# Kernel optimization log

Measured on AMD Instinct MI355X. Metric: run time of the kernel, lower is better.

Reference implementation:

```python
import jax, jax.numpy as jnp
import numpy as np

B, H, W = 4, 768, 768
K = 4096            # max zero-crossing points kept per sample (padded/masked)
UPDATE_SCALE = 1.0
DIST_THRESHOLD = 3.0
W_INJECT = 1.0
W_PIXEL = 1.0
EPS = 1e-8
BIG = 1e30          # stand-in for +inf distance of invalid gt points


def _make_sdf(radius, center, key):
    # signed distance to a circle + smooth low-frequency perturbation -> realistic SDF
    r = jnp.arange(H, dtype=jnp.float32)[:, None]
    c = jnp.arange(W, dtype=jnp.float32)[None, :]
    d = jnp.sqrt((r - center[0]) ** 2 + (c - center[1]) ** 2) - radius
    noise = jax.random.normal(key, (H // 32, W // 32), dtype=jnp.float32)
    noise = jax.image.resize(noise, (H, W), method='bilinear') * 2.0
    return d + noise


def setup_inputs() -> dict:
    key = jax.random.key(0)
    ks = jax.random.split(key, 2 * B)
    preds, gts = [], []
    for b in range(B):
        cr, cc = H / 2 + 10 * b, W / 2 - 7 * b
        preds.append(_make_sdf(240.0 + 3 * b, (cr, cc), ks[2 * b]))
        gts.append(_make_sdf(250.0 - 2 * b, (cr + 5, cc - 4), ks[2 * b + 1]))
    return {"pred_sdf": jnp.stack(preds), "gt_sdf": jnp.stack(gts)}


def extract_zc(sdf):
    """Padded zero-crossing extraction: returns (K,2) coords and (K,) valid mask."""
    v1, v2 = sdf[:-1, :], sdf[1:, :]
    mask_v = (v1 * v2) < 0
    alpha_v = jnp.abs(v1) / (jnp.abs(v1) + jnp.abs(v2) + EPS)
    rs_v = jnp.arange(H - 1, dtype=jnp.float32)[:, None] + alpha_v          # (H-1,W)
    cs_v = jnp.broadcast_to(jnp.arange(W, dtype=jnp.float32)[None, :], (H - 1, W))

    h1, h2 = sdf[:, :-1], sdf[:, 1:]
    mask_h = (h1 * h2) < 0
    alpha_h = jnp.abs(h1) / (jnp.abs(h1) + jnp.abs(h2) + EPS)
    rs_h = jnp.broadcast_to(jnp.arange(H, dtype=jnp.float32)[:, None], (H, W - 1))
    cs_h = jnp.arange(W - 1, dtype=jnp.float32)[None, :] + alpha_h          # (H,W-1)

    mask_z = sdf == 0
    rz = jnp.broadcast_to(jnp.arange(H, dtype=jnp.float32)[:, None], (H, W))
    cz = jnp.broadcast_to(jnp.arange(W, dtype=jnp.float32)[None, :], (H, W))

    pts = jnp.concatenate([
        jnp.stack([rz.ravel(), cz.ravel()], -1),
        jnp.stack([rs_v.ravel(), cs_v.ravel()], -1),
        jnp.stack([rs_h.ravel(), cs_h.ravel()], -1)], axis=0)               # (M,2)
    mask = jnp.concatenate([mask_z.ravel(), mask_v.ravel(), mask_h.ravel()])
    order = jnp.argsort(~mask)[:K]      # stable sort -> True (crossing) entries first
    return pts[order], mask[order]


def compute_normals(sdf):
    gr = jnp.zeros_like(sdf)
    gr = gr.at[1:-1].set(0.5 * (sdf[2:] - sdf[:-2]))
    gr = gr.at[0].set(sdf[1] - sdf[0]).at[-1].set(sdf[-1] - sdf[-2])
    gc = jnp.zeros_like(sdf)
    gc = gc.at[:, 1:-1].set(0.5 * (sdf[:, 2:] - sdf[:, :-2]))
    gc = gc.at[:, 0].set(sdf[:, 1] - sdf[:, 0]).at[:, -1].set(sdf[:, -1] - sdf[:, -2])
    return jnp.stack([gr, gc], -1)      # (H,W,2)


def _corner(coords):
    r, c = coords[:, 0], coords[:, 1]
    r0 = jnp.clip(jnp.floor(r).astype(jnp.int32), 0, H - 1)
    c0 = jnp.clip(jnp.floor(c).astype(jnp.int32), 0, W - 1)
    r1 = jnp.clip(r0 + 1, 0, H - 1)
    c1 = jnp.clip(c0 + 1, 0, W - 1)
    ar = r - r0.astype(jnp.float32)
    ac = c - c0.astype(jnp.float32)
    return r0, c0, r1, c1, ar, ac


def bilinear_sample(img, coords):
    r0, c0, r1, c1, ar, ac = _corner(coords)
    return (img[r0, c0] * (1 - ar) * (1 - ac) + img[r0, c1] * (1 - ar) * ac
            + img[r1, c0] * ar * (1 - ac) + img[r1, c1] * ar * ac)


def chamfer_grad(pred2d, pred_zc, valid_p, gt_zc, valid_g):
    normals = compute_normals(pred2d)
    r0, c0, r1, c1, ar, ac = _corner(pred_zc)
    n = (normals[r0, c0] * ((1 - ar) * (1 - ac))[:, None]
         + normals[r0, c1] * ((1 - ar) * ac)[:, None]
         + normals[r1, c0] * (ar * (1 - ac))[:, None]
         + normals[r1, c1] * (ar * ac)[:, None])
    n = n / (jnp.linalg.norm(n, axis=1, keepdims=True) + 1e-8)

    diff = gt_zc[None, :, :] - pred_zc[:, None, :]          # (Kp,Kg,2)
    dist = jnp.linalg.norm(diff, axis=-1)                   # (Kp,Kg)
    dist = jnp.where(valid_g[None, :], dist, BIG)
    idx = jnp.argmin(dist, axis=1)
    min_dist = jnp.take_along_axis(dist, idx[:, None], 1)[:, 0]
    mask = (min_dist <= DIST_THRESHOLD) & valid_p & jnp.any(valid_g)
    dir_vec = jnp.take_along_axis(diff, idx[:, None, None], 1)[:, 0, :]
    dot = (dir_vec * n).sum(1) * UPDATE_SCALE
    dot = jnp.where(mask, dot, 0.0)

    w00 = (1 - ar) * (1 - ac); w01 = (1 - ar) * ac
    w10 = ar * (1 - ac);       w11 = ar * ac
    flat = lambda rr, cc: rr * W + cc
    indices = jnp.concatenate([flat(r0, c0), flat(r0, c1), flat(r1, c0), flat(r1, c1)])
    contribs = jnp.concatenate([dot * w00, dot * w01, dot * w10, dot * w11])
    dflat = jnp.zeros(H * W, dtype=pred2d.dtype).at[indices].add(contribs)
    return dflat.reshape(H, W)


def _per_sample(pred2d, gt2d):
    gt_zc, valid_g = extract_zc(gt2d)
    # torch uses pred.detach() for zero-crossing locations
    pred_zc, valid_p = extract_zc(jax.lax.stop_gradient(pred2d))
    dSDF = chamfer_grad(pred2d, pred_zc, valid_p, gt_zc, valid_g)
    inject = jnp.sum(pred2d * jax.lax.stop_gradient(dSDF))
    pixel = jnp.sum(jnp.where(valid_p, bilinear_sample(pred2d, pred_zc), 0.0))
    return inject, pixel


def reference(pred_sdf, gt_sdf):
    inject, pixel = jax.vmap(_per_sample)(pred_sdf, gt_sdf)
    return W_INJECT * inject.mean() + W_PIXEL * pixel.mean()
```

## Files before the change

kernel.cpp:

```cpp
#include <hip/hip_runtime.h>
#include <climits>


typedef unsigned long long ull;

constexpr int B = 4, H = 768, W = 768, K = 4096;
constexpr int HW = H * W;
constexpr int NFIELD = 2 * B;
constexpr int BANDS = 256;
constexpr int WPR = W / 64;
constexpr int SEGW = 768 * WPR;
constexpr int MSTRIDE = 3 * SEGW;
constexpr int GSPLIT = 16;
constexpr int GRNG = K / GSPLIT;
constexpr int IBLK = K / 256;
constexpr int NDBLK = B * HW / 256;
constexpr int NBKT_S = 16;

constexpr size_t alignup(size_t x, size_t a) { return (x + a - 1) & ~(a - 1); }

constexpr size_t OFF_ACCP  = 0;
constexpr size_t OFF_BACC  = OFF_ACCP + sizeof(double) * 8 * 8;
constexpr size_t OFF_CNT   = OFF_BACC + sizeof(double) * 64 * 8;
constexpr size_t OFF_WCNT  = OFF_CNT + sizeof(int) * NFIELD;
constexpr size_t OFF_MASKS = alignup(OFF_WCNT + sizeof(int) * NFIELD * 768, 8);
constexpr size_t OFF_PTS   = OFF_MASKS + sizeof(ull) * NFIELD * MSTRIDE;
constexpr size_t OFF_NNKEY = OFF_PTS + sizeof(float2) * NFIELD * K;
constexpr size_t OFF_HEADS = alignup(OFF_NNKEY + sizeof(ull) * (size_t)B * K, 16);
constexpr size_t OFF_NXT   = OFF_HEADS + sizeof(int) * (size_t)B * HW;
constexpr size_t OFF_EVAL  = OFF_NXT + sizeof(int) * (size_t)B * 4 * K;
constexpr size_t OFF_DIRTY = OFF_EVAL + sizeof(float) * (size_t)B * 4 * K;
constexpr size_t WS_NEED   = OFF_DIRTY + sizeof(int) * NDBLK;

#define DEVFN __device__ __forceinline__

DEVFN float grad_r(const float* __restrict__ s, int r, int c) {
#pragma clang fp contract(off)
  if (r == 0)      return s[W + c] - s[c];
  if (r == H - 1)  return s[(H - 1) * W + c] - s[(H - 2) * W + c];
  return 0.5f * (s[(r + 1) * W + c] - s[(r - 1) * W + c]);
}
DEVFN float grad_c(const float* __restrict__ s, int r, int c) {
#pragma clang fp contract(off)
  if (c == 0)      return s[r * W + 1] - s[r * W];
  if (c == W - 1)  return s[r * W + W - 1] - s[r * W + W - 2];
  return 0.5f * (s[r * W + c + 1] - s[r * W + c - 1]);
}

DEVFN const float* field_sdf(const float* pred, const float* gt, int f) {
  return ((f & 1) ? gt : pred) + (size_t)(f >> 1) * HW;
}

__global__ __launch_bounds__(256) void k_count(const float* __restrict__ pred,
                                               const float* __restrict__ gt,
                                               ull* __restrict__ masks,
                                               int* __restrict__ wave_cnt,
                                               int* __restrict__ heads,
                                               int* __restrict__ dirty,
                                               ull* __restrict__ nnkey,
                                               double* __restrict__ bacc,
                                               double* __restrict__ accp) {
#pragma clang fp contract(off)
  int gtid = blockIdx.x * 256 + (int)threadIdx.x;
  int gsz = gridDim.x * 256;
  int4* h4 = (int4*)heads;
  for (int idx = gtid; idx < B * HW / 4; idx += gsz)
    h4[idx] = make_int4(-1, -1, -1, -1);
  for (int idx = gtid; idx < NDBLK; idx += gsz) dirty[idx] = 0;
  for (int idx = gtid; idx < B * K; idx += gsz) nnkey[idx] = ~0ull;
  if (gtid < 64) accp[gtid] = 0.0;
  if (gtid >= 64 && gtid < 64 + 512) bacc[gtid - 64] = 0.0;

  int f = blockIdx.x >> 6;
  int bb = blockIdx.x & 63;
  int wave = threadIdx.x >> 6, lane = threadIdx.x & 63;
  int band = bb * 4 + wave;
  int r0 = band * 3;
  const float* sdf = field_sdf(pred, gt, f);
  ull* mz = masks + (size_t)f * MSTRIDE;
  ull* mv = mz + SEGW;
  ull* mh = mv + SEGW;

  float cur[WPR], nxt[WPR];
#pragma unroll
  for (int i = 0; i < WPR; ++i) cur[i] = sdf[r0 * W + i * 64 + lane];
  int cz = 0, cv = 0, ch = 0;
  for (int rr = 0; rr < 3; ++rr) {
    int row = r0 + rr;
    bool hasNext = row < H - 1;
    if (hasNext) {
#pragma unroll
      for (int i = 0; i < WPR; ++i) nxt[i] = sdf[(row + 1) * W + i * 64 + lane];
    }
#pragma unroll
    for (int i = 0; i < WPR; ++i) {
      ull m = __ballot(cur[i] == 0.0f);
      if (lane == 0) mz[row * WPR + i] = m;
      cz += __popcll(m);
      float nb = __shfl_down(cur[i], 1);
      float nb2 = (i < WPR - 1) ? __shfl(cur[i + 1], 0) : 0.0f;
      if (lane == 63) nb = nb2;
      bool hp = (i * 64 + lane < W - 1) && (cur[i] * nb < 0.0f);
      m = __ballot(hp);
      if (lane == 0) mh[row * WPR + i] = m;
      ch += __popcll(m);
      if (hasNext) {
        m = __ballot(cur[i] * nxt[i] < 0.0f);
        if (lane == 0) mv[row * WPR + i] = m;
        cv += __popcll(m);
      }
    }
    if (hasNext) {
#pragma unroll
      for (int i = 0; i < WPR; ++i) cur[i] = nxt[i];
    }
  }
  if (lane == 0) {
    int* wc = wave_cnt + f * 768;
    wc[0 * BANDS + band] = cz;
    wc[1 * BANDS + band] = cv;
    wc[2 * BANDS + band] = ch;
  }
}

__global__ __launch_bounds__(256) void k_emit(const float* __restrict__ pred,
                                              const float* __restrict__ gt,
                                              const ull* __restrict__ masks,
                                              const int* __restrict__ wave_cnt,
                                              float2* __restrict__ pts,
                                              int* __restrict__ counts_raw) {
#pragma clang fp contract(off)
  int f = blockIdx.x / 192;
  int tb = blockIdx.x - f * 192;
  __shared__ int cnt_s[768];
  for (int t = threadIdx.x; t < 768; t += 256) cnt_s[t] = wave_cnt[f * 768 + t];
  __syncthreads();
  int wave = threadIdx.x >> 6, lane = threadIdx.x & 63;
  int task = tb * 4 + wave;
  int seg = task >> 8, band = task & 255;
  int a = 0;
  for (int idx = lane; idx < task; idx += 64) a += cnt_s[idx];
  for (int off = 32; off > 0; off >>= 1) a += __shfl_xor(a, off, 64);
  int base = a;
  if (tb == 0 && wave == 0) {
    int t2 = 0;
    for (int idx = lane; idx < 768; idx += 64) t2 += cnt_s[idx];
    for (int off = 32; off > 0; off >>= 1) t2 += __shfl_xor(t2, off, 64);
    if (lane == 0) counts_raw[f] = t2;
  }
  if (base >= K) return;
  const float* sdf = field_sdf(pred, gt, f);
  const ull* mseg = masks + (size_t)f * MSTRIDE + (size_t)seg * SEGW;
  float2* fp = pts + (size_t)f * K;
  int r0 = band * 3;
  for (int rr = 0; rr < 3; ++rr) {
    int row = r0 + rr;
    if (seg == 1 && row >= H - 1) break;
    for (int i = 0; i < WPR; ++i) {
      ull m = mseg[row * WPR + i];
      if (!m) continue;
      if ((m >> lane) & 1ull) {
        int c = i * 64 + lane;
        float pr, pc;
        if (seg == 0) {
          pr = (float)row; pc = (float)c;
        } else if (seg == 1) {
          float v1 = sdf[row * W + c], v2 = sdf[(row + 1) * W + c];
          float a1 = fabsf(v1), a2 = fabsf(v2);
          float alpha = a1 / ((a1 + a2) + 1e-8f);
          pr = (float)row + alpha; pc = (float)c;
        } else {
          float h1 = sdf[row * W + c], h2 = sdf[row * W + c + 1];
          float a1 = fabsf(h1), a2 = fabsf(h2);
          float alpha = a1 / ((a1 + a2) + 1e-8f);
          pr = (float)row; pc = (float)c + alpha;
        }
        int pos = base + __popcll(m & ((1ull << lane) - 1ull));
        if (pos < K) fp[pos] = make_float2(pr, pc);
      }
      base += __popcll(m);
      if (base >= K) { rr = 3; break; }
    }
  }
}

__global__ __launch_bounds__(256) void k_nn(const float2* __restrict__ pts,
                                            const int* __restrict__ counts_raw,
                                            ull* __restrict__ nnkey) {
#pragma clang fp contract(off)
  int b = blockIdx.x >> 8;
  int rem = blockIdx.x & 255;
  int ib = rem >> 4, ig = rem & 15;
  int tid = (int)threadIdx.x;
  int np_ = min(counts_raw[2 * b + 0], K);
  int ng  = min(counts_raw[2 * b + 1], K);
  int j0 = ig * GRNG;
  int n = min(GRNG, ng - j0);
  const float2* gp = pts + (size_t)(2 * b + 1) * K;

  __shared__ float2 tile[GRNG];
  __shared__ float smin[256], smax[256];
  float rmin = __builtin_inff(), rmax = -__builtin_inff();
  if (tid < n) {
    float2 g = gp[j0 + tid];
    tile[tid] = g;
    rmin = g.x; rmax = g.x;
  }
  smin[tid] = rmin; smax[tid] = rmax;
  __syncthreads();
  for (int s = 128; s > 0; s >>= 1) {
    if (tid < s) {
      smin[tid] = fminf(smin[tid], smin[tid + s]);
      smax[tid] = fmaxf(smax[tid], smax[tid + s]);
    }
    __syncthreads();
  }
  float gmin = smin[0] - 3.001f, gmax = smax[0] + 3.001f;

  int i = ib * 256 + tid;
  if (i >= np_ || n <= 0) return;
  float2 q = pts[(size_t)(2 * b) * K + i];
  float pr = q.x, pc = q.y;
  if (pr < gmin || pr > gmax) return;
  float best = __builtin_inff();
  unsigned bj = 0xffffffffu;
#pragma unroll 4
  for (int j = 0; j < n; ++j) {
    float dr = tile[j].x - pr;
    float dc = tile[j].y - pc;
    float sqf = fmaf(dr, dr, dc * dc);
    if (sqf <= 9.0001f) {
      float d = sqrtf((dr * dr) + (dc * dc));
      if (d < best) { best = d; bj = (unsigned)(j0 + j); }
    }
  }
  if (bj != 0xffffffffu)
    atomicMin(&nnkey[(size_t)b * K + i],
              ((ull)__float_as_uint(best) << 32) | bj);
}

__global__ __launch_bounds__(256) void k_post(const float* __restrict__ pred,
                                              const float2* __restrict__ pts,
                                              const int* __restrict__ counts_raw,
                                              const ull* __restrict__ nnkey,
                                              int* __restrict__ heads,
                                              int* __restrict__ nxt,
                                              float* __restrict__ eval,
                                              int* __restrict__ dirty,
                                              double* __restrict__ accp) {
#pragma clang fp contract(off)
  int b = blockIdx.x >> 4;
  int i = ((blockIdx.x & 15) << 8) + (int)threadIdx.x;
  const float* P = pred + (size_t)b * HW;
  int np_ = min(counts_raw[2 * b + 0], K);
  bool active = (i < np_);
  float sval = 0.0f;
  if (active) {
    ull key = nnkey[(size_t)b * K + i];
    float2 q = pts[(size_t)(2 * b) * K + i];
    float pr = q.x, pc = q.y;

    int r0 = (int)floorf(pr); r0 = r0 < 0 ? 0 : (r0 > H - 1 ? H - 1 : r0);
    int c0 = (int)floorf(pc); c0 = c0 < 0 ? 0 : (c0 > W - 1 ? W - 1 : c0);
    int r1 = (r0 + 1 > H - 1) ? H - 1 : r0 + 1;
    int c1 = (c0 + 1 > W - 1) ? W - 1 : c0 + 1;
    float ar = pr - (float)r0;
    float ac = pc - (float)c0;
    float omr = 1.0f - ar, omc = 1.0f - ac;
    float u00 = omr * omc, u01 = omr * ac, u10 = ar * omc, u11 = ar * ac;

    float v00 = P[r0 * W + c0], v01 = P[r0 * W + c1];
    float v10 = P[r1 * W + c0], v11 = P[r1 * W + c1];
    sval = (v00 * omr) * omc + (v01 * omr) * ac + (v10 * ar) * omc + (v11 * ar) * ac;

    float best = __uint_as_float((unsigned)(key >> 32));
    if (best <= 3.0f) {
      const float2* gp = pts + (size_t)(2 * b + 1) * K;
      float2 g = gp[(unsigned)(key & 0xffffffffu)];
      float grA = grad_r(P, r0, c0), grB = grad_r(P, r0, c1);
      float grC = grad_r(P, r1, c0), grD = grad_r(P, r1, c1);
      float gcA = grad_c(P, r0, c0), gcB = grad_c(P, r0, c1);
      float gcC = grad_c(P, r1, c0), gcD = grad_c(P, r1, c1);
      float n_r = ((grA * u00 + grB * u01) + grC * u10) + grD * u11;
      float n_c = ((gcA * u00 + gcB * u01) + gcC * u10) + gcD * u11;
      float nn = sqrtf((n_r * n_r) + (n_c * n_c));
      float den = nn + 1e-8f;
      float nrm_r = n_r / den, nrm_c = n_c / den;
      float dr = g.x - pr, dc = g.y - pc;
      float dot = (dr * nrm_r) + (dc * nrm_c);
      dot = dot * 1.0f;
      if (dot != 0.0f) {
        int px[4] = { r0 * W + c0, r0 * W + c1, r1 * W + c0, r1 * W + c1 };
        float cv[4] = { dot * u00, dot * u01, dot * u10, dot * u11 };
        int basee = b * 4 * K;
        for (int k2 = 0; k2 < 4; ++k2) {
          int e = k2 * K + i;
          eval[basee + e] = cv[k2];
          nxt[basee + e] = atomicExch(&heads[(size_t)b * HW + px[k2]], e);
          dirty[(b * HW + px[k2]) >> 8] = 1;
        }
      }
    }
  }
  __shared__ double red[256];
  red[threadIdx.x] = (double)sval;
  __syncthreads();
  for (int s = 128; s > 0; s >>= 1) {
    if ((int)threadIdx.x < s) red[threadIdx.x] += red[threadIdx.x + s];
    __syncthreads();
  }
  if (threadIdx.x == 0 && red[0] != 0.0)
    atomicAdd(&accp[(4 + b) * 8], red[0]);
}

__global__ __launch_bounds__(256) void k_gather(const float* __restrict__ pred,
                                                const int* __restrict__ heads,
                                                const int* __restrict__ nxt,
                                                const float* __restrict__ eval,
                                                const int* __restrict__ dirty,
                                                double* __restrict__ bacc) {
#pragma clang fp contract(off)
  if (!dirty[blockIdx.x]) return;
  int idx = blockIdx.x * 256 + (int)threadIdx.x;
  int b = idx / HW;
  float term = 0.0f;
  int h = heads[idx];
  if (h >= 0) {
    int base = b * 4 * K;
    float facc = 0.0f;
    int last = -1;
    for (;;) {
      int bestE = INT_MAX;
      for (int e = h; e >= 0; e = nxt[base + e])
        if (e > last && e < bestE) bestE = e;
      if (bestE == INT_MAX) break;
      facc = facc + eval[base + bestE];
      last = bestE;
    }
    term = pred[idx] * facc;
  }
  __shared__ double red[256];
  red[threadIdx.x] = (double)term;
  __syncthreads();
  for (int s = 128; s > 0; s >>= 1) {
    if ((int)threadIdx.x < s) red[threadIdx.x] += red[threadIdx.x + s];
    __syncthreads();
  }
  if (threadIdx.x == 0 && red[0] != 0.0)
    atomicAdd(&bacc[((b << 4) | ((int)blockIdx.x & (NBKT_S - 1))) * 8], red[0]);
}

__global__ __launch_bounds__(256) void k_final(const double* __restrict__ bacc,
                                               const double* __restrict__ accp,
                                               float* __restrict__ out) {
  __shared__ double sv[72];
  int tid = (int)threadIdx.x;
  if (tid < 64) sv[tid] = bacc[tid * 8];
  else if (tid < 72) sv[tid] = accp[(tid - 64) * 8];
  __syncthreads();
  if (tid == 0) {
    double mi = 0.0, mp = 0.0;
    for (int s = 0; s < 4; ++s) {
      for (int k2 = 0; k2 < NBKT_S; ++k2) mi += sv[s * NBKT_S + k2];
      mp += sv[64 + 4 + s];
    }
    out[0] = (float)(mi * 0.25 + mp * 0.25);
  }
}

extern "C" void kernel_launch(void* const* d_in, const int* in_sizes, int n_in,
                              void* d_out, int out_size, void* d_ws, size_t ws_size,
                              hipStream_t stream) {
  const float* pred = (const float*)d_in[0];
  const float* gt   = (const float*)d_in[1];
  float* out = (float*)d_out;
  char* ws = (char*)d_ws;

  double* accp       = (double*)(ws + OFF_ACCP);
  double* bacc       = (double*)(ws + OFF_BACC);
  int*    counts_raw = (int*)(ws + OFF_CNT);
  int*    wave_cnt   = (int*)(ws + OFF_WCNT);
  ull*    masks      = (ull*)(ws + OFF_MASKS);
  float2* pts        = (float2*)(ws + OFF_PTS);
  ull*    nnkey      = (ull*)(ws + OFF_NNKEY);
  int*    heads      = (int*)(ws + OFF_HEADS);
  int*    nxt        = (int*)(ws + OFF_NXT);
  float*  eval       = (float*)(ws + OFF_EVAL);
  int*    dirty      = (int*)(ws + OFF_DIRTY);

  (void)in_sizes; (void)n_in; (void)out_size; (void)ws_size;

  k_count<<<dim3(NFIELD * 64), dim3(256), 0, stream>>>(pred, gt, masks, wave_cnt,
                                                       heads, dirty, nnkey,
                                                       bacc, accp);
  k_emit<<<dim3(NFIELD * 192), dim3(256), 0, stream>>>(pred, gt, masks, wave_cnt,
                                                       pts, counts_raw);
  k_nn<<<dim3(B * IBLK * GSPLIT), dim3(256), 0, stream>>>(pts, counts_raw, nnkey);
  k_post<<<dim3(B * IBLK), dim3(256), 0, stream>>>(pred, pts, counts_raw, nnkey,
                                                   heads, nxt, eval, dirty, accp);
  k_gather<<<dim3(NDBLK), dim3(256), 0, stream>>>(pred, heads, nxt, eval, dirty,
                                                  bacc);
  k_final<<<dim3(1), dim3(256), 0, stream>>>(bacc, accp, out);
}
```

Measured before the change: 79.71 us.

## Replace brute-force NN with band-indexed spatial search fused into post kernel

Records the per-band prefix offsets from the emit stage so that gt points, already ordered by row band, can be looked up by row range. Each pred point then scans only the gt points in the bands within distance 3, and this search is fused with the post-processing kernel. That removes the separate all-pairs NN kernel, the nnkey buffer and its init, and the 64-bit atomicMin. The pixel-term reduction moves to wavefront shuffles with bucketed atomics. The trade-off is per-thread serial loops of uneven length in small 64-thread blocks, which gives low parallelism and irregular global loads.

```diff
diff --git a/kernel.cpp b/kernel.cpp
--- a/kernel.cpp
+++ b/kernel.cpp
@@ -11,22 +11,18 @@
 constexpr int WPR = W / 64;
 constexpr int SEGW = 768 * WPR;
 constexpr int MSTRIDE = 3 * SEGW;
-constexpr int GSPLIT = 16;
-constexpr int GRNG = K / GSPLIT;
-constexpr int IBLK = K / 256;
 constexpr int NDBLK = B * HW / 256;
 constexpr int NBKT_S = 16;
 
 constexpr size_t alignup(size_t x, size_t a) { return (x + a - 1) & ~(a - 1); }
 
-constexpr size_t OFF_ACCP  = 0;
-constexpr size_t OFF_BACC  = OFF_ACCP + sizeof(double) * 8 * 8;
-constexpr size_t OFF_CNT   = OFF_BACC + sizeof(double) * 64 * 8;
-constexpr size_t OFF_WCNT  = OFF_CNT + sizeof(int) * NFIELD;
+constexpr size_t OFF_BACC  = 0;
+constexpr size_t OFF_CNT   = OFF_BACC + sizeof(double) * 128 * 8;
+constexpr size_t OFF_TBASE = OFF_CNT + sizeof(int) * NFIELD;
+constexpr size_t OFF_WCNT  = OFF_TBASE + sizeof(int) * NFIELD * 768;
 constexpr size_t OFF_MASKS = alignup(OFF_WCNT + sizeof(int) * NFIELD * 768, 8);
 constexpr size_t OFF_PTS   = OFF_MASKS + sizeof(ull) * NFIELD * MSTRIDE;
-constexpr size_t OFF_NNKEY = OFF_PTS + sizeof(float2) * NFIELD * K;
-constexpr size_t OFF_HEADS = alignup(OFF_NNKEY + sizeof(ull) * (size_t)B * K, 16);
+constexpr size_t OFF_HEADS = alignup(OFF_PTS + sizeof(float2) * NFIELD * K, 16);
 constexpr size_t OFF_NXT   = OFF_HEADS + sizeof(int) * (size_t)B * HW;
 constexpr size_t OFF_EVAL  = OFF_NXT + sizeof(int) * (size_t)B * 4 * K;
 constexpr size_t OFF_DIRTY = OFF_EVAL + sizeof(float) * (size_t)B * 4 * K;
@@ -57,9 +53,7 @@
                                                int* __restrict__ wave_cnt,
                                                int* __restrict__ heads,
                                                int* __restrict__ dirty,
-                                               ull* __restrict__ nnkey,
-                                               double* __restrict__ bacc,
-                                               double* __restrict__ accp) {
+                                               double* __restrict__ bacc) {
 #pragma clang fp contract(off)
   int gtid = blockIdx.x * 256 + (int)threadIdx.x;
   int gsz = gridDim.x * 256;
@@ -67,9 +61,7 @@
   for (int idx = gtid; idx < B * HW / 4; idx += gsz)
     h4[idx] = make_int4(-1, -1, -1, -1);
   for (int idx = gtid; idx < NDBLK; idx += gsz) dirty[idx] = 0;
-  for (int idx = gtid; idx < B * K; idx += gsz) nnkey[idx] = ~0ull;
-  if (gtid < 64) accp[gtid] = 0.0;
-  if (gtid >= 64 && gtid < 64 + 512) bacc[gtid - 64] = 0.0;
+  if (gtid < 1024) bacc[gtid] = 0.0;
 
   int f = blockIdx.x >> 6;
   int bb = blockIdx.x & 63;
@@ -128,7 +120,8 @@
                                               const ull* __restrict__ masks,
                                               const int* __restrict__ wave_cnt,
                                               float2* __restrict__ pts,
-                                              int* __restrict__ counts_raw) {
+                                              int* __restrict__ counts_raw,
+                                              int* __restrict__ task_base) {
 #pragma clang fp contract(off)
   int f = blockIdx.x / 192;
   int tb = blockIdx.x - f * 192;
@@ -142,6 +135,7 @@
   for (int idx = lane; idx < task; idx += 64) a += cnt_s[idx];
   for (int off = 32; off > 0; off >>= 1) a += __shfl_xor(a, off, 64);
   int base = a;
+  if (lane == 0) task_base[f * 768 + task] = base;
   if (tb == 0 && wave == 0) {
     int t2 = 0;
     for (int idx = lane; idx < 768; idx += 64) t2 += cnt_s[idx];
@@ -184,82 +178,58 @@
   }
 }
 
-__global__ __launch_bounds__(256) void k_nn(const float2* __restrict__ pts,
-                                            const int* __restrict__ counts_raw,
-                                            ull* __restrict__ nnkey) {
-#pragma clang fp contract(off)
-  int b = blockIdx.x >> 8;
-  int rem = blockIdx.x & 255;
-  int ib = rem >> 4, ig = rem & 15;
-  int tid = (int)threadIdx.x;
+__global__ __launch_bounds__(64) void k_nn_post(const float* __restrict__ pred,
+                                                const float2* __restrict__ pts,
+                                                const int* __restrict__ counts_raw,
+                                                const int* __restrict__ task_base,
+                                                int* __restrict__ heads,
+                                                int* __restrict__ nxt,
+                                                float* __restrict__ eval,
+                                                int* __restrict__ dirty,
+                                                double* __restrict__ bacc) {
+#pragma clang fp contract(off)
+  int b = blockIdx.x >> 6;
+  int g = blockIdx.x & 63;
+  int i = (g << 6) + (int)threadIdx.x;
   int np_ = min(counts_raw[2 * b + 0], K);
-  int ng  = min(counts_raw[2 * b + 1], K);
-  int j0 = ig * GRNG;
-  int n = min(GRNG, ng - j0);
+  int ngt = counts_raw[2 * b + 1];
+  int ng = min(ngt, K);
   const float2* gp = pts + (size_t)(2 * b + 1) * K;
-
-  __shared__ float2 tile[GRNG];
-  __shared__ float smin[256], smax[256];
-  float rmin = __builtin_inff(), rmax = -__builtin_inff();
-  if (tid < n) {
-    float2 g = gp[j0 + tid];
-    tile[tid] = g;
-    rmin = g.x; rmax = g.x;
-  }
-  smin[tid] = rmin; smax[tid] = rmax;
-  __syncthreads();
-  for (int s = 128; s > 0; s >>= 1) {
-    if (tid < s) {
-      smin[tid] = fminf(smin[tid], smin[tid + s]);
-      smax[tid] = fmaxf(smax[tid], smax[tid + s]);
-    }
-    __syncthreads();
-  }
-  float gmin = smin[0] - 3.001f, gmax = smax[0] + 3.001f;
-
-  int i = ib * 256 + tid;
-  if (i >= np_ || n <= 0) return;
-  float2 q = pts[(size_t)(2 * b) * K + i];
-  float pr = q.x, pc = q.y;
-  if (pr < gmin || pr > gmax) return;
+  const int* tbg = task_base + (2 * b + 1) * 768;
+  const float* P = pred + (size_t)b * HW;
+
+  bool active = (i < np_);
+  float pr = 0.0f, pc = 0.0f;
+  if (active) { float2 q = pts[(size_t)(2 * b) * K + i]; pr = q.x; pc = q.y; }
+
   float best = __builtin_inff();
-  unsigned bj = 0xffffffffu;
-#pragma unroll 4
-  for (int j = 0; j < n; ++j) {
-    float dr = tile[j].x - pr;
-    float dc = tile[j].y - pc;
-    float sqf = fmaf(dr, dr, dc * dc);
-    if (sqf <= 9.0001f) {
-      float d = sqrtf((dr * dr) + (dc * dc));
-      if (d < best) { best = d; bj = (unsigned)(j0 + j); }
-    }
-  }
-  if (bj != 0xffffffffu)
-    atomicMin(&nnkey[(size_t)b * K + i],
-              ((ull)__float_as_uint(best) << 32) | bj);
-}
-
-__global__ __launch_bounds__(256) void k_post(const float* __restrict__ pred,
-                                              const float2* __restrict__ pts,
-                                              const int* __restrict__ counts_raw,
-                                              const ull* __restrict__ nnkey,
-                                              int* __restrict__ heads,
-                                              int* __restrict__ nxt,
-                                              float* __restrict__ eval,
-                                              int* __restrict__ dirty,
-                                              double* __restrict__ accp) {
-#pragma clang fp contract(off)
-  int b = blockIdx.x >> 4;
-  int i = ((blockIdx.x & 15) << 8) + (int)threadIdx.x;
-  const float* P = pred + (size_t)b * HW;
-  int np_ = min(counts_raw[2 * b + 0], K);
-  bool active = (i < np_);
+  int bj = -1;
+  if (active && ng > 0) {
+    int blo = (int)floorf((pr - 4.01f) * (1.0f / 3.0f));
+    int bhi = (int)floorf((pr + 3.01f) * (1.0f / 3.0f));
+    blo = blo < 0 ? 0 : blo;
+    bhi = bhi > 255 ? 255 : bhi;
+    for (int seg = 0; seg < 3; ++seg) {
+      int tlo = seg * 256 + blo, thi = seg * 256 + bhi;
+      int jlo = tbg[tlo];
+      int jhi = (thi >= 767) ? ngt : tbg[thi + 1];
+      jlo = jlo < ng ? jlo : ng;
+      jhi = jhi < ng ? jhi : ng;
+      for (int j = jlo; j < jhi; ++j) {
+        float2 g2 = gp[j];
+        float dr = g2.x - pr;
+        float dc = g2.y - pc;
+        float sqf = fmaf(dr, dr, dc * dc);
+        if (sqf <= 9.0001f) {
+          float d = sqrtf((dr * dr) + (dc * dc));
+          if (d < best) { best = d; bj = j; }
+        }
+      }
+    }
+  }
+
   float sval = 0.0f;
   if (active) {
-    ull key = nnkey[(size_t)b * K + i];
-    float2 q = pts[(size_t)(2 * b) * K + i];
-    float pr = q.x, pc = q.y;
-
     int r0 = (int)floorf(pr); r0 = r0 < 0 ? 0 : (r0 > H - 1 ? H - 1 : r0);
     int c0 = (int)floorf(pc); c0 = c0 < 0 ? 0 : (c0 > W - 1 ? W - 1 : c0);
     int r1 = (r0 + 1 > H - 1) ? H - 1 : r0 + 1;
@@ -273,10 +243,8 @@
     float v10 = P[r1 * W + c0], v11 = P[r1 * W + c1];
     sval = (v00 * omr) * omc + (v01 * omr) * ac + (v10 * ar) * omc + (v11 * ar) * ac;
 
-    float best = __uint_as_float((unsigned)(key >> 32));
     if (best <= 3.0f) {
-      const float2* gp = pts + (size_t)(2 * b + 1) * K;
-      float2 g = gp[(unsigned)(key & 0xffffffffu)];
+      float2 g2 = gp[bj];
       float grA = grad_r(P, r0, c0), grB = grad_r(P, r0, c1);
       float grC = grad_r(P, r1, c0), grD = grad_r(P, r1, c1);
       float gcA = grad_c(P, r0, c0), gcB = grad_c(P, r0, c1);
@@ -286,7 +254,7 @@
       float nn = sqrtf((n_r * n_r) + (n_c * n_c));
       float den = nn + 1e-8f;
       float nrm_r = n_r / den, nrm_c = n_c / den;
-      float dr = g.x - pr, dc = g.y - pc;
+      float dr = g2.x - pr, dc = g2.y - pc;
       float dot = (dr * nrm_r) + (dc * nrm_c);
       dot = dot * 1.0f;
       if (dot != 0.0f) {
@@ -302,15 +270,10 @@
       }
     }
   }
-  __shared__ double red[256];
-  red[threadIdx.x] = (double)sval;
-  __syncthreads();
-  for (int s = 128; s > 0; s >>= 1) {
-    if ((int)threadIdx.x < s) red[threadIdx.x] += red[threadIdx.x + s];
-    __syncthreads();
-  }
-  if (threadIdx.x == 0 && red[0] != 0.0)
-    atomicAdd(&accp[(4 + b) * 8], red[0]);
+  double sd = (double)sval;
+  for (int off = 32; off > 0; off >>= 1) sd += __shfl_down(sd, off, 64);
+  if (threadIdx.x == 0 && sd != 0.0)
+    atomicAdd(&bacc[(size_t)(64 + (b << 4) + (g & (NBKT_S - 1))) * 8], sd);
 }
 
 __global__ __launch_bounds__(256) void k_gather(const float* __restrict__ pred,
@@ -347,23 +310,23 @@
     __syncthreads();
   }
   if (threadIdx.x == 0 && red[0] != 0.0)
-    atomicAdd(&bacc[((b << 4) | ((int)blockIdx.x & (NBKT_S - 1))) * 8], red[0]);
+    atomicAdd(&bacc[(size_t)((b << 4) | ((int)blockIdx.x & (NBKT_S - 1))) * 8],
+              red[0]);
 }
 
 __global__ __launch_bounds__(256) void k_final(const double* __restrict__ bacc,
-                                               const double* __restrict__ accp,
                                                float* __restrict__ out) {
-  __shared__ double sv[72];
+  __shared__ double sv[128];
   int tid = (int)threadIdx.x;
-  if (tid < 64) sv[tid] = bacc[tid * 8];
-  else if (tid < 72) sv[tid] = accp[(tid - 64) * 8];
+  if (tid < 128) sv[tid] = bacc[(size_t)tid * 8];
   __syncthreads();
   if (tid == 0) {
     double mi = 0.0, mp = 0.0;
-    for (int s = 0; s < 4; ++s) {
-      for (int k2 = 0; k2 < NBKT_S; ++k2) mi += sv[s * NBKT_S + k2];
-      mp += sv[64 + 4 + s];
-    }
+    for (int s = 0; s < B; ++s)
+      for (int k2 = 0; k2 < NBKT_S; ++k2) {
+        mi += sv[s * NBKT_S + k2];
+        mp += sv[64 + s * NBKT_S + k2];
+      }
     out[0] = (float)(mi * 0.25 + mp * 0.25);
   }
 }
@@ -376,13 +339,12 @@
   float* out = (float*)d_out;
   char* ws = (char*)d_ws;
 
-  double* accp       = (double*)(ws + OFF_ACCP);
   double* bacc       = (double*)(ws + OFF_BACC);
   int*    counts_raw = (int*)(ws + OFF_CNT);
+  int*    task_base  = (int*)(ws + OFF_TBASE);
   int*    wave_cnt   = (int*)(ws + OFF_WCNT);
   ull*    masks      = (ull*)(ws + OFF_MASKS);
   float2* pts        = (float2*)(ws + OFF_PTS);
-  ull*    nnkey      = (ull*)(ws + OFF_NNKEY);
   int*    heads      = (int*)(ws + OFF_HEADS);
   int*    nxt        = (int*)(ws + OFF_NXT);
   float*  eval       = (float*)(ws + OFF_EVAL);
@@ -391,14 +353,12 @@
   (void)in_sizes; (void)n_in; (void)out_size; (void)ws_size;
 
   k_count<<<dim3(NFIELD * 64), dim3(256), 0, stream>>>(pred, gt, masks, wave_cnt,
-                                                       heads, dirty, nnkey,
-                                                       bacc, accp);
+                                                       heads, dirty, bacc);
   k_emit<<<dim3(NFIELD * 192), dim3(256), 0, stream>>>(pred, gt, masks, wave_cnt,
-                                                       pts, counts_raw);
-  k_nn<<<dim3(B * IBLK * GSPLIT), dim3(256), 0, stream>>>(pts, counts_raw, nnkey);
-  k_post<<<dim3(B * IBLK), dim3(256), 0, stream>>>(pred, pts, counts_raw, nnkey,
-                                                   heads, nxt, eval, dirty, accp);
+                                                       pts, counts_raw, task_base);
+  k_nn_post<<<dim3(B * 64), dim3(64), 0, stream>>>(pred, pts, counts_raw, task_base,
+                                                   heads, nxt, eval, dirty, bacc);
   k_gather<<<dim3(NDBLK), dim3(256), 0, stream>>>(pred, heads, nxt, eval, dirty,
                                                   bacc);
-  k_final<<<dim3(1), dim3(256), 0, stream>>>(bacc, accp, out);
-}
+  k_final<<<dim3(1), dim3(256), 0, stream>>>(bacc, out);
+}
```

Result: no change. 79.97 us (+0.3%).
